# Kernel tuning notes

Hardware: AMD Instinct MI355X
Metric: run time of the kernel (lower is better)

Reference implementation:

```python
import jax, jax.numpy as jnp
import numpy as np

N, M, E, DIM, H = 50000, 50000, 640000, 128, 8
DH = DIM // H
EPS = 1e-5

def _prelu(x, alpha):
    return jnp.where(x >= 0, x, alpha * x)

def setup_inputs() -> dict:
    key0 = jax.random.key(0)
    ks = jax.random.split(key0, 12)
    s = 1.0 / np.sqrt(DIM)
    return {
        "query": jax.random.normal(ks[0], (N, DIM), jnp.float32),
        "key": jax.random.normal(ks[1], (M, DIM), jnp.float32),
        "value": jax.random.normal(ks[2], (M, DIM), jnp.float32),
        "query_idx": jax.random.randint(ks[3], (E,), 0, N),
        "key_idx": jax.random.randint(ks[4], (E,), 0, M),
        "Wq": jax.random.normal(ks[5], (DIM, DIM), jnp.float32) * s,
        "bq": jnp.zeros((DIM,), jnp.float32),
        "Wk": jax.random.normal(ks[6], (DIM, DIM), jnp.float32) * s,
        "bk": jnp.zeros((DIM,), jnp.float32),
        "Wv": jax.random.normal(ks[7], (DIM, DIM), jnp.float32) * s,
        "bv": jnp.zeros((DIM,), jnp.float32),
        "Wp": jax.random.normal(ks[8], (DIM, DIM), jnp.float32) * s,
        "bp": jnp.zeros((DIM,), jnp.float32),
        "a": jax.random.normal(ks[9], (1, H, DH), jnp.float32) * 0.1,
        "alpha": jnp.full((1,), 0.25, jnp.float32),
        "gamma": jnp.ones((DIM,), jnp.float32),
        "beta": jnp.zeros((DIM,), jnp.float32),
    }

def reference(query, key, value, query_idx, key_idx, Wq, bq, Wk, bk, Wv, bv, Wp, bp, a, alpha, gamma, beta):
    n = query.shape[0]
    # projections (node-level, then gather per edge; linear commutes with gather)
    Qq = query @ Wq + bq            # [N, DIM]
    Kq = query @ Wk + bk            # [N, DIM] (self-attn key)
    Kk = key @ Wk + bk              # [M, DIM]
    Vq = query @ Wv + bv            # [N, DIM]
    Vv = value @ Wv + bv            # [M, DIM]
    # self-attention score per query node: [N, H, 1]
    attn_qq = (a * _prelu(Qq + Kq, alpha).reshape(n, H, DH)).sum(-1, keepdims=True)
    # per-edge additive attention score: [E, H, 1]
    e_feat = _prelu(Qq[query_idx] + Kk[key_idx], alpha)
    attn_e = (a * e_feat.reshape(-1, H, DH)).sum(-1, keepdims=True)
    # stable softmax over irregular query groups (include self)
    max_attn = jax.lax.stop_gradient(attn_qq.at[query_idx].max(attn_e))
    exp_qq = jnp.exp(attn_qq - max_attn)                 # [N, H, 1]
    exp_e = jnp.exp(attn_e - max_attn[query_idx])        # [E, H, 1]
    denom = exp_qq.at[query_idx].add(exp_e)              # [N, H, 1]
    denom = jnp.where(denom == 0, 1.0, denom)
    # weighted value scatter-sum (value_idx == key_idx)
    msg = exp_qq * Vq.reshape(n, H, DH)
    msg = msg.at[query_idx].add(exp_e * Vv[key_idx].reshape(-1, H, DH))
    out = (msg / denom).reshape(n, DIM) @ Wp + bp
    res = query + out
    mu = res.mean(-1, keepdims=True)
    var = res.var(-1, keepdims=True)
    return gamma * (res - mu) / jnp.sqrt(var + EPS) + beta
```

## Files before the change

### kernel.cpp

```cpp
#include <hip/hip_runtime.h>
#include <math.h>

#define DIM 128
#define NH 8
#define LN_EPS 1e-5f
#define NEGINF -3.0e38f

using bf16x8 = __attribute__((ext_vector_type(8))) short;
using f32x4  = __attribute__((ext_vector_type(4))) float;

__device__ __forceinline__ float prelu_f(float x, float al) { return x >= 0.f ? x : al * x; }

__device__ __forceinline__ short f2bf(float f) {
    unsigned u = __float_as_uint(f);
    unsigned r = (u + 0x7fffu + ((u >> 16) & 1u)) >> 16;
    return (short)r;
}
__device__ __forceinline__ float bflo(unsigned u) { return __uint_as_float(u << 16); }
__device__ __forceinline__ float bfhi(unsigned u) { return __uint_as_float(u & 0xffff0000u); }
__device__ __forceinline__ float bfs(short s) { return __uint_as_float(((unsigned)(unsigned short)s) << 16); }

__device__ __forceinline__ unsigned cvt_pk_bf16(float lo, float hi) {
    unsigned r;
    asm("v_cvt_pk_bf16_f32 %0, %1, %2" : "=v"(r) : "v"(lo), "v"(hi));
    return r;
}

__device__ __forceinline__ float swz_xor1(float x) {
    return __int_as_float(__builtin_amdgcn_ds_swizzle(__float_as_int(x), 0x041F));
}
__device__ __forceinline__ float swz_xor16(float x) {
    return __int_as_float(__builtin_amdgcn_ds_swizzle(__float_as_int(x), 0x401F));
}
__device__ __forceinline__ float swz_xor32(float x) {
    return __shfl_xor(x, 32);
}

__global__ __launch_bounds__(256) void setup_kernel(
    const float* __restrict__ W0, const float* __restrict__ W1,
    const float* __restrict__ W2, const float* __restrict__ W3,
    short* __restrict__ P0, short* __restrict__ P1,
    short* __restrict__ P2, short* __restrict__ P3)
{
    const int id = blockIdx.x * 256 + threadIdx.x;
    const int mat = id >> 11;
    const int rem = id & 2047;
    const int ks = rem >> 9;
    const int ct = (rem >> 6) & 7;
    const int lane = rem & 63;
    const int lr = lane & 15, lg = lane >> 4;
    const float* W = mat == 0 ? W0 : mat == 1 ? W1 : mat == 2 ? W2 : W3;
    short* P = mat == 0 ? P0 : mat == 1 ? P1 : mat == 2 ? P2 : P3;
    short v[8];
    #pragma unroll
    for (int r = 0; r < 8; ++r)
        v[r] = f2bf(W[(ks * 32 + lg * 8 + r) * DIM + ct * 16 + lr]);
    *(bf16x8*)&P[(size_t)((ks * 8 + ct) * 64 + lane) * 8] = *(bf16x8*)v;
}

__global__ __launch_bounds__(256) void proj_all_mfma(
    const float* __restrict__ query,
    const float* __restrict__ key, const float* __restrict__ value,
    const short* __restrict__ Wqp, const short* __restrict__ Wkp, const short* __restrict__ Wvp,
    const float* __restrict__ bq, const float* __restrict__ bk, const float* __restrict__ bv,
    const float* __restrict__ avec, const float* __restrict__ alpha_p,
    short* __restrict__ QV16, float* __restrict__ attnqq8,
    short* __restrict__ KV16,
    const int* __restrict__ qidx, int* __restrict__ counts, int E,
    int N, int M, int nb)
{
    __shared__ short wbuf[16384];
    __shared__ short tile[4][16][132];
    const int wid = threadIdx.x >> 6, lane = threadIdx.x & 63;
    const int lr = lane & 15, lg = lane >> 4;
    const int mb = (M + 63) >> 6;

    if ((int)blockIdx.x >= nb + mb) {
        const int b = (int)blockIdx.x - nb - mb;
        for (int e = b * 256 + threadIdx.x; e < E; e += 1024 * 256)
            atomicAdd(&counts[qidx[e]], 1);
        return;
    }

    #define STAGE_W(Wsrc)                                                     \
        {                                                                     \
            _Pragma("unroll")                                                 \
            for (int j = 0; j < 8; ++j) {                                     \
                const int cch = (int)threadIdx.x + j * 256;                   \
                *(bf16x8*)&wbuf[cch * 8] = *(const bf16x8*)&(Wsrc)[cch * 8];  \
            }                                                                 \
        }

    if ((int)blockIdx.x < nb) {
        const int row0 = ((int)blockIdx.x * 4 + wid) * 16;
        const int arow = row0 + lr;
        const bool rowok = arow < N;

        bf16x8 afrag[4];
        #pragma unroll
        for (int ks = 0; ks < 4; ++ks) {
            float t[8] = {0.f,0.f,0.f,0.f,0.f,0.f,0.f,0.f};
            if (rowok) {
                *(float4*)&t[0] = *(const float4*)&query[(size_t)arow * DIM + ks * 32 + lg * 8];
                *(float4*)&t[4] = *(const float4*)&query[(size_t)arow * DIM + ks * 32 + lg * 8 + 4];
            }
            union { bf16x8 v; unsigned u[4]; } a;
            a.u[0] = cvt_pk_bf16(t[0], t[1]);
            a.u[1] = cvt_pk_bf16(t[2], t[3]);
            a.u[2] = cvt_pk_bf16(t[4], t[5]);
            a.u[3] = cvt_pk_bf16(t[6], t[7]);
            afrag[ks] = a.v;
        }
        const float al = alpha_p[0];
        unsigned* qvout = (unsigned*)QV16;

        STAGE_W(Wqp);
        __syncthreads();
        #pragma unroll 2
        for (int ct = 0; ct < 8; ++ct) {
            f32x4 aq = (f32x4)0.f;
            #pragma unroll
            for (int ks = 0; ks < 4; ++ks)
                aq = __builtin_amdgcn_mfma_f32_16x16x32_bf16(afrag[ks],
                        *(const bf16x8*)&wbuf[((ks * 8 + ct) * 64 + lane) * 8], aq, 0, 0, 0);
            const int col = ct * 16 + lr;
            const float bqv = bq[col];
            #pragma unroll
            for (int r = 0; r < 4; ++r)
                tile[wid][lg * 4 + r][col] = (short)cvt_pk_bf16(aq[r] + bqv, 0.f);
        }
        #pragma unroll
        for (int rr = 0; rr < 16; ++rr) {
            const int grow = row0 + rr;
            if (grow < N) {
                const short2 pr = *(const short2*)&tile[wid][rr][lane * 2];
                qvout[(size_t)grow * 128 + lane] =
                    (unsigned)(unsigned short)pr.x | ((unsigned)(unsigned short)pr.y << 16);
            }
        }
        __syncthreads();

        STAGE_W(Wkp);
        __syncthreads();
        #pragma unroll 2
        for (int ct = 0; ct < 8; ++ct) {
            f32x4 ak = (f32x4)0.f;
            #pragma unroll
            for (int ks = 0; ks < 4; ++ks)
                ak = __builtin_amdgcn_mfma_f32_16x16x32_bf16(afrag[ks],
                        *(const bf16x8*)&wbuf[((ks * 8 + ct) * 64 + lane) * 8], ak, 0, 0, 0);
            const int col = ct * 16 + lr;
            const float bkv = bk[col], av = avec[col];
            #pragma unroll
            for (int r = 0; r < 4; ++r) {
                const int row = lg * 4 + r;
                const float qv = bfs(tile[wid][row][col]);
                const float kv = ak[r] + bkv;
                float part = av * prelu_f(qv + kv, al);
                part += swz_xor1(part);
                const int grow = row0 + row;
                if ((lr & 1) == 0 && grow < N)
                    attnqq8[(size_t)grow * 64 + ct * 8 + (lr >> 1)] = part;
            }
        }
        __syncthreads();

        STAGE_W(Wvp);
        __syncthreads();
        #pragma unroll 2
        for (int ct = 0; ct < 8; ++ct) {
            f32x4 acv = (f32x4)0.f;
            #pragma unroll
            for (int ks = 0; ks < 4; ++ks)
                acv = __builtin_amdgcn_mfma_f32_16x16x32_bf16(afrag[ks],
                        *(const bf16x8*)&wbuf[((ks * 8 + ct) * 64 + lane) * 8], acv, 0, 0, 0);
            const int col = ct * 16 + lr;
            const float bvv = bv[col];
            #pragma unroll
            for (int r = 0; r < 4; ++r)
                tile[wid][lg * 4 + r][col] = (short)cvt_pk_bf16(acv[r] + bvv, 0.f);
        }
        #pragma unroll
        for (int rr = 0; rr < 16; ++rr) {
            const int grow = row0 + rr;
            if (grow < N) {
                const short2 pr = *(const short2*)&tile[wid][rr][lane * 2];
                qvout[(size_t)grow * 128 + 64 + lane] =
                    (unsigned)(unsigned short)pr.x | ((unsigned)(unsigned short)pr.y << 16);
            }
        }
    } else {
        const int row0 = (((int)blockIdx.x - nb) * 4 + wid) * 16;
        const int arow = row0 + lr;
        const bool rowok = arow < M;
        unsigned* kvout = (unsigned*)KV16;

        bf16x8 afK[4], afV[4];
        #pragma unroll
        for (int ks = 0; ks < 4; ++ks) {
            float tk[8] = {0.f,0.f,0.f,0.f,0.f,0.f,0.f,0.f};
            float tv[8] = {0.f,0.f,0.f,0.f,0.f,0.f,0.f,0.f};
            if (rowok) {
                *(float4*)&tk[0] = *(const float4*)&key[(size_t)arow * DIM + ks * 32 + lg * 8];
                *(float4*)&tk[4] = *(const float4*)&key[(size_t)arow * DIM + ks * 32 + lg * 8 + 4];
                *(float4*)&tv[0] = *(const float4*)&value[(size_t)arow * DIM + ks * 32 + lg * 8];
                *(float4*)&tv[4] = *(const float4*)&value[(size_t)arow * DIM + ks * 32 + lg * 8 + 4];
            }
            union { bf16x8 v; unsigned u[4]; } a, b;
            a.u[0] = cvt_pk_bf16(tk[0], tk[1]);
            a.u[1] = cvt_pk_bf16(tk[2], tk[3]);
            a.u[2] = cvt_pk_bf16(tk[4], tk[5]);
            a.u[3] = cvt_pk_bf16(tk[6], tk[7]);
            b.u[0] = cvt_pk_bf16(tv[0], tv[1]);
            b.u[1] = cvt_pk_bf16(tv[2], tv[3]);
            b.u[2] = cvt_pk_bf16(tv[4], tv[5]);
            b.u[3] = cvt_pk_bf16(tv[6], tv[7]);
            afK[ks] = a.v; afV[ks] = b.v;
        }

        STAGE_W(Wkp);
        __syncthreads();
        #pragma unroll 2
        for (int ct = 0; ct < 8; ++ct) {
            f32x4 ack = (f32x4)0.f;
            #pragma unroll
            for (int ks = 0; ks < 4; ++ks)
                ack = __builtin_amdgcn_mfma_f32_16x16x32_bf16(afK[ks],
                        *(const bf16x8*)&wbuf[((ks * 8 + ct) * 64 + lane) * 8], ack, 0, 0, 0);
            const int col = ct * 16 + lr;
            const float bkv = bk[col];
            #pragma unroll
            for (int r = 0; r < 4; ++r)
                tile[wid][lg * 4 + r][col] = (short)cvt_pk_bf16(ack[r] + bkv, 0.f);
        }
        #pragma unroll
        for (int rr = 0; rr < 16; ++rr) {
            const int grow = row0 + rr;
            if (grow < M) {
                const short2 pr = *(const short2*)&tile[wid][rr][lane * 2];
                kvout[(size_t)grow * 128 + lane] =
                    (unsigned)(unsigned short)pr.x | ((unsigned)(unsigned short)pr.y << 16);
            }
        }
        __syncthreads();

        STAGE_W(Wvp);
        __syncthreads();
        #pragma unroll 2
        for (int ct = 0; ct < 8; ++ct) {
            f32x4 acv = (f32x4)0.f;
            #pragma unroll
            for (int ks = 0; ks < 4; ++ks)
                acv = __builtin_amdgcn_mfma_f32_16x16x32_bf16(afV[ks],
                        *(const bf16x8*)&wbuf[((ks * 8 + ct) * 64 + lane) * 8], acv, 0, 0, 0);
            const int col = ct * 16 + lr;
            const float bvv = bv[col];
            #pragma unroll
            for (int r = 0; r < 4; ++r)
                tile[wid][lg * 4 + r][col] = (short)cvt_pk_bf16(acv[r] + bvv, 0.f);
        }
        #pragma unroll
        for (int rr = 0; rr < 16; ++rr) {
            const int grow = row0 + rr;
            if (grow < M) {
                const short2 pr = *(const short2*)&tile[wid][rr][lane * 2];
                kvout[(size_t)grow * 128 + 64 + lane] =
                    (unsigned)(unsigned short)pr.x | ((unsigned)(unsigned short)pr.y << 16);
            }
        }
    }
    #undef STAGE_W
}

__global__ __launch_bounds__(256) void scan1_kernel(const int* __restrict__ counts,
                                                    int* __restrict__ bsum, int N)
{
    __shared__ int sh[256];
    int i = blockIdx.x * 256 + threadIdx.x;
    sh[threadIdx.x] = (i < N) ? counts[i] : 0;
    __syncthreads();
    #pragma unroll
    for (int off = 128; off; off >>= 1) {
        if (threadIdx.x < off) sh[threadIdx.x] += sh[threadIdx.x + off];
        __syncthreads();
    }
    if (threadIdx.x == 0) bsum[blockIdx.x] = sh[0];
}

__global__ __launch_bounds__(256) void scan2_kernel(const int* __restrict__ bsum,
                                                    int* __restrict__ boff, int B)
{
    int t = threadIdx.x;
    if (B > 256) {
        if (t == 0) { int run = 0; for (int i = 0; i < B; ++i) { int v = bsum[i]; boff[i] = run; run += v; } }
        return;
    }
    __shared__ int sh[256];
    int v = (t < B) ? bsum[t] : 0;
    sh[t] = v;
    __syncthreads();
    for (int off = 1; off < 256; off <<= 1) {
        int x = (t >= off) ? sh[t - off] : 0;
        __syncthreads();
        sh[t] += x;
        __syncthreads();
    }
    if (t < B) boff[t] = sh[t] - v;
}

__global__ __launch_bounds__(256) void scan3_kernel(const int* __restrict__ counts,
                                                    const int* __restrict__ boff,
                                                    int* __restrict__ offsets,
                                                    int* __restrict__ cursor,
                                                    int N, int E)
{
    __shared__ int sh[256];
    int t = threadIdx.x;
    int i = blockIdx.x * 256 + t;
    int v = (i < N) ? counts[i] : 0;
    sh[t] = v;
    __syncthreads();
    for (int off = 1; off < 256; off <<= 1) {
        int x = (t >= off) ? sh[t - off] : 0;
        __syncthreads();
        sh[t] += x;
        __syncthreads();
    }
    int base = boff[blockIdx.x];
    if (i < N) {
        int o = base + sh[t] - v;
        offsets[i] = o;
        cursor[i] = o;
    }
    if (i == 0) offsets[N] = E;
}

__global__ void fill_kernel(const int* __restrict__ qidx, const int* __restrict__ kidx,
                            int* __restrict__ cursor, int* __restrict__ ksorted, int E)
{
    for (int e = blockIdx.x * blockDim.x + threadIdx.x; e < E; e += gridDim.x * blockDim.x) {
        int q = qidx[e];
        int pos = atomicAdd(&cursor[q], 1);
        ksorted[pos] = kidx[e];
    }
}

__global__ __launch_bounds__(256) void edge_agg_kernel(
    const short* __restrict__ QV16, const float* __restrict__ attnqq8,
    const short* __restrict__ KV16,
    const int* __restrict__ ksorted, const int* __restrict__ offsets,
    const float* __restrict__ avec, const float* __restrict__ alpha_p,
    short* __restrict__ msgn16, int N)
{
    const int lane = threadIdx.x & 63;
    const int wid  = threadIdx.x >> 6;
    const int e    = lane >> 4;
    const int sub  = lane & 15;
    const int h    = sub >> 1;

    const float al = alpha_p[0];
    const float r  = (1.f - al) / (1.f + al);
    const float s1 = (1.f + al) * 0.5f;

    float c[8];
    {
        const float4 a0 = *(const float4*)&avec[sub * 8];
        const float4 a1 = *(const float4*)&avec[sub * 8 + 4];
        c[0] = a0.x * s1; c[1] = a0.y * s1; c[2] = a0.z * s1; c[3] = a0.w * s1;
        c[4] = a1.x * s1; c[5] = a1.y * s1; c[6] = a1.z * s1; c[7] = a1.w * s1;
    }

    const char* KVb = (const char*)KV16;
    const unsigned subB = (unsigned)(sub * 16);
    const int wavesTotal = gridDim.x * 4;

    for (int n = blockIdx.x * 4 + wid; n < N; n += wavesTotal) {
        float q[8];
        {
            unsigned qd[4];
            *(uint4*)qd = *(const uint4*)&QV16[(size_t)n * 256 + sub * 8];
            #pragma unroll
            for (int j = 0; j < 4; ++j) { q[2*j] = bflo(qd[j]); q[2*j+1] = bfhi(qd[j]); }
        }

        float acc[8];
        float den;
        if (e == 0) {
            float sself;
            {
                const float4 a4 = *(const float4*)&attnqq8[(size_t)n * 64 + h * 8];
                const float4 b4 = *(const float4*)&attnqq8[(size_t)n * 64 + h * 8 + 4];
                sself = ((a4.x + a4.y) + (a4.z + a4.w)) + ((b4.x + b4.y) + (b4.z + b4.w));
            }
            const float ws = __expf(sself);
            unsigned vdi[4];
            *(uint4*)vdi = *(const uint4*)&QV16[(size_t)n * 256 + 128 + sub * 8];
            #pragma unroll
            for (int j = 0; j < 4; ++j) {
                acc[2*j]   = ws * bflo(vdi[j]);
                acc[2*j+1] = ws * bfhi(vdi[j]);
            }
            den = ws;
        } else {
            #pragma unroll
            for (int d = 0; d < 8; ++d) acc[d] = 0.f;
            den = 0.f;
        }

        const int p0 = offsets[n];
        const int p1 = offsets[n + 1];
        const int T  = (p1 - p0 + 3) >> 2;

        #define ROWLOAD(kd_, vd_, ki_)                                        \
            {                                                                 \
                const unsigned ob = (unsigned)(ki_) * 512u + subB;            \
                *(uint4*)(kd_) = *(const uint4*)(KVb + ob);                   \
                *(uint4*)(vd_) = *(const uint4*)(KVb + ob + 256);             \
            }

        unsigned kdA[4], vdA[4], kdB[4], vdB[4];
        unsigned kdC[4], vdC[4], kdD[4], vdD[4];
        bool vA, vB, vC, vD;
        int kiA, kiB, kiC, kiD;

        {
            int i0 = p0 + e,      i1 = p0 + 4 + e;
            int i2 = p0 + 8 + e,  i3 = p0 + 12 + e;
            vA = i0 < p1; vB = i1 < p1; vC = i2 < p1; vD = i3 < p1;
            const int k0 = vA ? ksorted[i0] : 0;
            const int k1 = vB ? ksorted[i1] : 0;
            const int k2 = vC ? ksorted[i2] : 0;
            const int k3 = vD ? ksorted[i3] : 0;
            ROWLOAD(kdA, vdA, k0); ROWLOAD(kdB, vdB, k1);
            ROWLOAD(kdC, vdC, k2); ROWLOAD(kdD, vdD, k3);
            int j0 = p0 + 16 + e, j1 = p0 + 20 + e;
            int j2 = p0 + 24 + e, j3 = p0 + 28 + e;
            kiA = (j0 < p1) ? ksorted[j0] : 0;
            kiB = (j1 < p1) ? ksorted[j1] : 0;
            kiC = (j2 < p1) ? ksorted[j2] : 0;
            kiD = (j3 < p1) ? ksorted[j3] : 0;
        }

        #define COMPUTE(kd_, vd_, vflag)                                      \
            {                                                                 \
                float sp = 0.f;                                               \
                _Pragma("unroll")                                             \
                for (int j = 0; j < 4; ++j) {                                 \
                    const float x0 = q[2*j]   + bflo(kd_[j]);                 \
                    const float x1 = q[2*j+1] + bfhi(kd_[j]);                 \
                    const float t0 = fmaf(r, __builtin_fabsf(x0), x0);        \
                    const float t1 = fmaf(r, __builtin_fabsf(x1), x1);        \
                    sp = fmaf(c[2*j], t0, sp);                                \
                    sp = fmaf(c[2*j+1], t1, sp);                              \
                }                                                             \
                const float sf = sp + swz_xor1(sp);                           \
                const float s = (vflag) ? sf : NEGINF;                        \
                const float w = __expf(s);                 \
                den += w;                                                     \
                _Pragma("unroll")                                             \
                for (int j = 0; j < 4; ++j) {                                 \
                    acc[2*j]   = fmaf(w, bflo(vd_[j]), acc[2*j]);             \
                    acc[2*j+1] = fmaf(w, bfhi(vd_[j]), acc[2*j+1]);           \
                }                                                             \
            }

        #define RELOAD(kd_, vd_, vflag, ki_, st4, st8)                        \
            {                                                                 \
                vflag = (p0 + (st4) * 4 + e) < p1;                            \
                ROWLOAD(kd_, vd_, ki_);                                       \
                const int fi = p0 + (st8) * 4 + e;                            \
                ki_ = (fi < p1) ? ksorted[fi] : 0;                            \
            }

        #pragma unroll 1
        for (int t = 0; t < T; t += 4) {
            COMPUTE(kdA, vdA, vA); RELOAD(kdA, vdA, vA, kiA, t + 4, t + 8);
            COMPUTE(kdB, vdB, vB); RELOAD(kdB, vdB, vB, kiB, t + 5, t + 9);
            COMPUTE(kdC, vdC, vC); RELOAD(kdC, vdC, vC, kiC, t + 6, t + 10);
            COMPUTE(kdD, vdD, vD); RELOAD(kdD, vdD, vD, kiD, t + 7, t + 11);
        }
        #undef COMPUTE
        #undef RELOAD
        #undef ROWLOAD

        {
            den += swz_xor16(den);
            #pragma unroll
            for (int d = 0; d < 8; ++d) acc[d] += swz_xor16(acc[d]);
            den += swz_xor32(den);
            #pragma unroll
            for (int d = 0; d < 8; ++d) acc[d] += swz_xor32(acc[d]);
        }

        if (e == 0) {
            const float inv = 1.f / den;
            unsigned u[4];
            #pragma unroll
            for (int j = 0; j < 4; ++j)
                u[j] = cvt_pk_bf16(acc[2*j] * inv, acc[2*j+1] * inv);
            *(uint4*)&msgn16[(size_t)n * DIM + sub * 8] = *(uint4*)u;
        }
    }
}

__global__ __launch_bounds__(256) void out_ln_mfma(
    const short* __restrict__ msgn16, const short* __restrict__ Wpp,
    const float* __restrict__ bp, const float* __restrict__ query,
    const float* __restrict__ gamma, const float* __restrict__ beta,
    float* __restrict__ out, int N)
{
    __shared__ float ys[64][130];
    const int wid = threadIdx.x >> 6, lane = threadIdx.x & 63;
    const int rowbase = blockIdx.x * 64;
    const int row0 = rowbase + wid * 16;
    const int lr = lane & 15, lg = lane >> 4;

    if (row0 < N) {
        bf16x8 afrag[4];
        const int arow = row0 + lr;
        const bool rowok = arow < N;
        #pragma unroll
        for (int ks = 0; ks < 4; ++ks) {
            if (rowok)
                afrag[ks] = *(const bf16x8*)&msgn16[(size_t)arow * DIM + ks * 32 + lg * 8];
            else {
                bf16x8 z;
                #pragma unroll
                for (int j = 0; j < 8; ++j) z[j] = 0;
                afrag[ks] = z;
            }
        }
        #pragma unroll 2
        for (int ct = 0; ct < 8; ++ct) {
            f32x4 acc = (f32x4)0.f;
            #pragma unroll
            for (int ks = 0; ks < 4; ++ks) {
                const size_t bo = (size_t)((ks * 8 + ct) * 64 + lane) * 8;
                acc = __builtin_amdgcn_mfma_f32_16x16x32_bf16(afrag[ks], *(const bf16x8*)&Wpp[bo], acc, 0, 0, 0);
            }
            const int col = ct * 16 + lr;
            const float bpv = bp[col];
            #pragma unroll
            for (int r = 0; r < 4; ++r)
                ys[wid * 16 + lg * 4 + r][col] = acc[r] + bpv;
        }
    }
    __syncthreads();

    for (int rr = 0; rr < 16; ++rr) {
        const int r = wid * 16 + rr;
        const int grow = rowbase + r;
        if (grow >= N) break;
        const float y1 = ys[r][lane], y2 = ys[r][lane + 64];
        const float q1 = query[(size_t)grow * DIM + lane];
        const float q2 = query[(size_t)grow * DIM + lane + 64];
        const float r1 = y1 + q1, r2 = y2 + q2;
        float s = r1 + r2;
        float ss = r1 * r1 + r2 * r2;
        #pragma unroll
        for (int off = 32; off; off >>= 1) {
            s += __shfl_xor(s, off);
            ss += __shfl_xor(ss, off);
        }
        const float mu = s * (1.f / DIM);
        const float var = ss * (1.f / DIM) - mu * mu;
        const float rstd = rsqrtf(var + LN_EPS);
        out[(size_t)grow * DIM + lane] = gamma[lane] * (r1 - mu) * rstd + beta[lane];
        out[(size_t)grow * DIM + lane + 64] = gamma[lane + 64] * (r2 - mu) * rstd + beta[lane + 64];
    }
}

extern "C" void kernel_launch(void* const* d_in, const int* in_sizes, int n_in,
                              void* d_out, int out_size, void* d_ws, size_t ws_size,
                              hipStream_t stream) {
    const float* query = (const float*)d_in[0];
    const float* key   = (const float*)d_in[1];
    const float* value = (const float*)d_in[2];
    const int* query_idx = (const int*)d_in[3];
    const int* key_idx   = (const int*)d_in[4];
    const float* Wq = (const float*)d_in[5];
    const float* bq = (const float*)d_in[6];
    const float* Wk = (const float*)d_in[7];
    const float* bk = (const float*)d_in[8];
    const float* Wv = (const float*)d_in[9];
    const float* bv = (const float*)d_in[10];
    const float* Wp = (const float*)d_in[11];
    const float* bp = (const float*)d_in[12];
    const float* avec  = (const float*)d_in[13];
    const float* alpha = (const float*)d_in[14];
    const float* gamma = (const float*)d_in[15];
    const float* beta  = (const float*)d_in[16];
    float* out = (float*)d_out;

    const int N = in_sizes[0] / DIM;
    const int M = in_sizes[1] / DIM;
    const int E = in_sizes[3];

    float* f = (float*)d_ws;
    float* attnqq8 = f; f += (size_t)N * 64;
    short* sp = (short*)f;
    short* QV16 = sp;   sp += (size_t)N * 256;
    short* KV16 = sp;   sp += (size_t)M * 256;
    short* msgn16 = sp; sp += (size_t)N * DIM;
    short* Wqp = sp;    sp += DIM * DIM;
    short* Wkp = sp;    sp += DIM * DIM;
    short* Wvp = sp;    sp += DIM * DIM;
    short* Wpp = sp;    sp += DIM * DIM;
    int* ip = (int*)(((size_t)sp + 15) & ~(size_t)15);
    int* counts  = ip;  ip += N;
    int* offsets = ip;  ip += N + 1;
    int* cursor  = ip;  ip += N;
    int* bsum    = ip;  ip += 4096;
    int* boff    = ip;  ip += 4096;
    int* ksorted = ip;  ip += E;

    const int B = (N + 255) / 256;
    const int nb = (N + 63) / 64;
    const int mb = (M + 63) / 64;

    hipMemsetAsync(counts, 0, (size_t)N * sizeof(int), stream);

    setup_kernel<<<32, 256, 0, stream>>>(Wq, Wk, Wv, Wp, Wqp, Wkp, Wvp, Wpp);

    proj_all_mfma<<<nb + mb + 1024, 256, 0, stream>>>(
        query, key, value, Wqp, Wkp, Wvp, bq, bk, bv, avec, alpha,
        QV16, attnqq8, KV16, query_idx, counts, E, N, M, nb);

    scan1_kernel<<<B, 256, 0, stream>>>(counts, bsum, N);
    scan2_kernel<<<1, 256, 0, stream>>>(bsum, boff, B);
    scan3_kernel<<<B, 256, 0, stream>>>(counts, boff, offsets, cursor, N, E);
    fill_kernel<<<1024, 256, 0, stream>>>(query_idx, key_idx, cursor, ksorted, E);

    edge_agg_kernel<<<2048, 256, 0, stream>>>(
        QV16, attnqq8, KV16, ksorted, offsets, avec, alpha, msgn16, N);

    out_ln_mfma<<<(N + 63) / 64, 256, 0, stream>>>(
        msgn16, Wpp, bp, query, gamma, beta, out, N);
}
```

Baseline: 192.1 us.

## Persistent projection blocks with per-block weight staging; move count atomics to setup

The projection kernel now runs a fixed grid of 384+384 persistent blocks. Each block stages a weight matrix into LDS once and loops over many 64-row tiles, where previously every tile restaged all three matrices. The query-side Wq·Wk self-attention score now writes the Kq projection to a scratch buffer (msgn16, reused before edge_agg writes it) and reads it back in the Q pass. The edge-count atomics move into the setup kernel, and the projection launch moves after the scan/fill kernels. This reduces weight staging traffic but reloads the input rows once per weight pass and adds a global scratch round trip.

```diff
diff --git a/kernel.cpp b/kernel.cpp
--- a/kernel.cpp
+++ b/kernel.cpp
@@ -18,7 +18,7 @@
 }
 __device__ __forceinline__ float bflo(unsigned u) { return __uint_as_float(u << 16); }
 __device__ __forceinline__ float bfhi(unsigned u) { return __uint_as_float(u & 0xffff0000u); }
-__device__ __forceinline__ float bfs(short s) { return __uint_as_float(((unsigned)(unsigned short)s) << 16); }
+__device__ __forceinline__ float bfus(unsigned short s) { return __uint_as_float(((unsigned)s) << 16); }
 
 __device__ __forceinline__ unsigned cvt_pk_bf16(float lo, float hi) {
     unsigned r;
@@ -40,22 +40,29 @@
     const float* __restrict__ W0, const float* __restrict__ W1,
     const float* __restrict__ W2, const float* __restrict__ W3,
     short* __restrict__ P0, short* __restrict__ P1,
-    short* __restrict__ P2, short* __restrict__ P3)
-{
-    const int id = blockIdx.x * 256 + threadIdx.x;
-    const int mat = id >> 11;
-    const int rem = id & 2047;
-    const int ks = rem >> 9;
-    const int ct = (rem >> 6) & 7;
-    const int lane = rem & 63;
-    const int lr = lane & 15, lg = lane >> 4;
-    const float* W = mat == 0 ? W0 : mat == 1 ? W1 : mat == 2 ? W2 : W3;
-    short* P = mat == 0 ? P0 : mat == 1 ? P1 : mat == 2 ? P2 : P3;
-    short v[8];
-    #pragma unroll
-    for (int r = 0; r < 8; ++r)
-        v[r] = f2bf(W[(ks * 32 + lg * 8 + r) * DIM + ct * 16 + lr]);
-    *(bf16x8*)&P[(size_t)((ks * 8 + ct) * 64 + lane) * 8] = *(bf16x8*)v;
+    short* __restrict__ P2, short* __restrict__ P3,
+    const int* __restrict__ qidx, int* __restrict__ counts, int E)
+{
+    if (blockIdx.x < 32) {
+        const int id = blockIdx.x * 256 + threadIdx.x;
+        const int mat = id >> 11;
+        const int rem = id & 2047;
+        const int ks = rem >> 9;
+        const int ct = (rem >> 6) & 7;
+        const int lane = rem & 63;
+        const int lr = lane & 15, lg = lane >> 4;
+        const float* W = mat == 0 ? W0 : mat == 1 ? W1 : mat == 2 ? W2 : W3;
+        short* P = mat == 0 ? P0 : mat == 1 ? P1 : mat == 2 ? P2 : P3;
+        short v[8];
+        #pragma unroll
+        for (int r = 0; r < 8; ++r)
+            v[r] = f2bf(W[(ks * 32 + lg * 8 + r) * DIM + ct * 16 + lr]);
+        *(bf16x8*)&P[(size_t)((ks * 8 + ct) * 64 + lane) * 8] = *(bf16x8*)v;
+    } else {
+        const int b = blockIdx.x - 32;
+        for (int e = b * 256 + threadIdx.x; e < E; e += 1024 * 256)
+            atomicAdd(&counts[qidx[e]], 1);
+    }
 }
 
 __global__ __launch_bounds__(256) void proj_all_mfma(
@@ -65,22 +72,15 @@
     const float* __restrict__ bq, const float* __restrict__ bk, const float* __restrict__ bv,
     const float* __restrict__ avec, const float* __restrict__ alpha_p,
     short* __restrict__ QV16, float* __restrict__ attnqq8,
-    short* __restrict__ KV16,
-    const int* __restrict__ qidx, int* __restrict__ counts, int E,
-    int N, int M, int nb)
+    short* __restrict__ KV16, short* __restrict__ Kscr,
+    int N, int M, int QB, int KB)
 {
     __shared__ short wbuf[16384];
     __shared__ short tile[4][16][132];
     const int wid = threadIdx.x >> 6, lane = threadIdx.x & 63;
     const int lr = lane & 15, lg = lane >> 4;
-    const int mb = (M + 63) >> 6;
-
-    if ((int)blockIdx.x >= nb + mb) {
-        const int b = (int)blockIdx.x - nb - mb;
-        for (int e = b * 256 + threadIdx.x; e < E; e += 1024 * 256)
-            atomicAdd(&counts[qidx[e]], 1);
-        return;
-    }
+    const int nTN = (N + 63) >> 6;
+    const int nTM = (M + 63) >> 6;
 
     #define STAGE_W(Wsrc)                                                     \
         {                                                                     \
@@ -91,185 +91,196 @@
             }                                                                 \
         }
 
-    if ((int)blockIdx.x < nb) {
-        const int row0 = ((int)blockIdx.x * 4 + wid) * 16;
-        const int arow = row0 + lr;
-        const bool rowok = arow < N;
-
-        bf16x8 afrag[4];
-        #pragma unroll
-        for (int ks = 0; ks < 4; ++ks) {
-            float t[8] = {0.f,0.f,0.f,0.f,0.f,0.f,0.f,0.f};
-            if (rowok) {
-                *(float4*)&t[0] = *(const float4*)&query[(size_t)arow * DIM + ks * 32 + lg * 8];
-                *(float4*)&t[4] = *(const float4*)&query[(size_t)arow * DIM + ks * 32 + lg * 8 + 4];
-            }
-            union { bf16x8 v; unsigned u[4]; } a;
-            a.u[0] = cvt_pk_bf16(t[0], t[1]);
-            a.u[1] = cvt_pk_bf16(t[2], t[3]);
-            a.u[2] = cvt_pk_bf16(t[4], t[5]);
-            a.u[3] = cvt_pk_bf16(t[6], t[7]);
-            afrag[ks] = a.v;
-        }
+    #define LOAD_AFRAG(src, limit)                                            \
+        {                                                                     \
+            const int arow = row0 + lr;                                       \
+            const bool rowok = arow < (limit);                                \
+            _Pragma("unroll")                                                 \
+            for (int ks = 0; ks < 4; ++ks) {                                  \
+                float t_[8] = {0.f,0.f,0.f,0.f,0.f,0.f,0.f,0.f};              \
+                if (rowok) {                                                  \
+                    *(float4*)&t_[0] = *(const float4*)&(src)[(size_t)arow * DIM + ks * 32 + lg * 8];     \
+                    *(float4*)&t_[4] = *(const float4*)&(src)[(size_t)arow * DIM + ks * 32 + lg * 8 + 4]; \
+                }                                                             \
+                union { bf16x8 v; unsigned u[4]; } a_;                        \
+                a_.u[0] = cvt_pk_bf16(t_[0], t_[1]);                          \
+                a_.u[1] = cvt_pk_bf16(t_[2], t_[3]);                          \
+                a_.u[2] = cvt_pk_bf16(t_[4], t_[5]);                          \
+                a_.u[3] = cvt_pk_bf16(t_[6], t_[7]);                          \
+                afrag[ks] = a_.v;                                             \
+            }                                                                 \
+        }
+
+    if ((int)blockIdx.x < QB) {
         const float al = alpha_p[0];
         unsigned* qvout = (unsigned*)QV16;
+        unsigned* kscro = (unsigned*)Kscr;
+        bf16x8 afrag[4];
+
+        STAGE_W(Wkp);
+        __syncthreads();
+        for (int t = blockIdx.x; t < nTN; t += QB) {
+            const int row0 = t * 64 + wid * 16;
+            LOAD_AFRAG(query, N);
+            #pragma unroll 2
+            for (int ct = 0; ct < 8; ++ct) {
+                f32x4 ak = (f32x4)0.f;
+                #pragma unroll
+                for (int ks = 0; ks < 4; ++ks)
+                    ak = __builtin_amdgcn_mfma_f32_16x16x32_bf16(afrag[ks],
+                            *(const bf16x8*)&wbuf[((ks * 8 + ct) * 64 + lane) * 8], ak, 0, 0, 0);
+                const int col = ct * 16 + lr;
+                const float bkv = bk[col];
+                #pragma unroll
+                for (int r = 0; r < 4; ++r)
+                    tile[wid][lg * 4 + r][col] = (short)cvt_pk_bf16(ak[r] + bkv, 0.f);
+            }
+            #pragma unroll
+            for (int rr = 0; rr < 16; ++rr) {
+                const int grow = row0 + rr;
+                if (grow < N) {
+                    const short2 pr = *(const short2*)&tile[wid][rr][lane * 2];
+                    kscro[(size_t)grow * 64 + lane] =
+                        (unsigned)(unsigned short)pr.x | ((unsigned)(unsigned short)pr.y << 16);
+                }
+            }
+        }
+        __syncthreads();
 
         STAGE_W(Wqp);
         __syncthreads();
-        #pragma unroll 2
-        for (int ct = 0; ct < 8; ++ct) {
-            f32x4 aq = (f32x4)0.f;
-            #pragma unroll
-            for (int ks = 0; ks < 4; ++ks)
-                aq = __builtin_amdgcn_mfma_f32_16x16x32_bf16(afrag[ks],
-                        *(const bf16x8*)&wbuf[((ks * 8 + ct) * 64 + lane) * 8], aq, 0, 0, 0);
-            const int col = ct * 16 + lr;
-            const float bqv = bq[col];
-            #pragma unroll
-            for (int r = 0; r < 4; ++r)
-                tile[wid][lg * 4 + r][col] = (short)cvt_pk_bf16(aq[r] + bqv, 0.f);
-        }
-        #pragma unroll
-        for (int rr = 0; rr < 16; ++rr) {
-            const int grow = row0 + rr;
-            if (grow < N) {
-                const short2 pr = *(const short2*)&tile[wid][rr][lane * 2];
-                qvout[(size_t)grow * 128 + lane] =
-                    (unsigned)(unsigned short)pr.x | ((unsigned)(unsigned short)pr.y << 16);
-            }
-        }
-        __syncthreads();
+        for (int t = blockIdx.x; t < nTN; t += QB) {
+            const int row0 = t * 64 + wid * 16;
+            LOAD_AFRAG(query, N);
+            #pragma unroll 2
+            for (int ct = 0; ct < 8; ++ct) {
+                f32x4 aq = (f32x4)0.f;
+                #pragma unroll
+                for (int ks = 0; ks < 4; ++ks)
+                    aq = __builtin_amdgcn_mfma_f32_16x16x32_bf16(afrag[ks],
+                            *(const bf16x8*)&wbuf[((ks * 8 + ct) * 64 + lane) * 8], aq, 0, 0, 0);
+                const int col = ct * 16 + lr;
+                const float bqv = bq[col], av = avec[col];
+                #pragma unroll
+                for (int r = 0; r < 4; ++r) {
+                    const int row = lg * 4 + r;
+                    const int grow = row0 + row;
+                    const float qv = aq[r] + bqv;
+                    const float kvb = (grow < N)
+                        ? bfus(((const unsigned short*)Kscr)[(size_t)grow * 128 + col]) : 0.f;
+                    float part = av * prelu_f(qv + kvb, al);
+                    part += swz_xor1(part);
+                    if ((lr & 1) == 0 && grow < N)
+                        attnqq8[(size_t)grow * 64 + ct * 8 + (lr >> 1)] = part;
+                    tile[wid][row][col] = (short)cvt_pk_bf16(qv, 0.f);
+                }
+            }
+            #pragma unroll
+            for (int rr = 0; rr < 16; ++rr) {
+                const int grow = row0 + rr;
+                if (grow < N) {
+                    const short2 pr = *(const short2*)&tile[wid][rr][lane * 2];
+                    qvout[(size_t)grow * 128 + lane] =
+                        (unsigned)(unsigned short)pr.x | ((unsigned)(unsigned short)pr.y << 16);
+                }
+            }
+        }
+        __syncthreads();
+
+        STAGE_W(Wvp);
+        __syncthreads();
+        for (int t = blockIdx.x; t < nTN; t += QB) {
+            const int row0 = t * 64 + wid * 16;
+            LOAD_AFRAG(query, N);
+            #pragma unroll 2
+            for (int ct = 0; ct < 8; ++ct) {
+                f32x4 acv = (f32x4)0.f;
+                #pragma unroll
+                for (int ks = 0; ks < 4; ++ks)
+                    acv = __builtin_amdgcn_mfma_f32_16x16x32_bf16(afrag[ks],
+                            *(const bf16x8*)&wbuf[((ks * 8 + ct) * 64 + lane) * 8], acv, 0, 0, 0);
+                const int col = ct * 16 + lr;
+                const float bvv = bv[col];
+                #pragma unroll
+                for (int r = 0; r < 4; ++r)
+                    tile[wid][lg * 4 + r][col] = (short)cvt_pk_bf16(acv[r] + bvv, 0.f);
+            }
+            #pragma unroll
+            for (int rr = 0; rr < 16; ++rr) {
+                const int grow = row0 + rr;
+                if (grow < N) {
+                    const short2 pr = *(const short2*)&tile[wid][rr][lane * 2];
+                    qvout[(size_t)grow * 128 + 64 + lane] =
+                        (unsigned)(unsigned short)pr.x | ((unsigned)(unsigned short)pr.y << 16);
+                }
+            }
+        }
+    } else {
+        const int b = (int)blockIdx.x - QB;
+        unsigned* kvout = (unsigned*)KV16;
+        bf16x8 afrag[4];
 
         STAGE_W(Wkp);
         __syncthreads();
-        #pragma unroll 2
-        for (int ct = 0; ct < 8; ++ct) {
-            f32x4 ak = (f32x4)0.f;
-            #pragma unroll
-            for (int ks = 0; ks < 4; ++ks)
-                ak = __builtin_amdgcn_mfma_f32_16x16x32_bf16(afrag[ks],
-                        *(const bf16x8*)&wbuf[((ks * 8 + ct) * 64 + lane) * 8], ak, 0, 0, 0);
-            const int col = ct * 16 + lr;
-            const float bkv = bk[col], av = avec[col];
-            #pragma unroll
-            for (int r = 0; r < 4; ++r) {
-                const int row = lg * 4 + r;
-                const float qv = bfs(tile[wid][row][col]);
-                const float kv = ak[r] + bkv;
-                float part = av * prelu_f(qv + kv, al);
-                part += swz_xor1(part);
-                const int grow = row0 + row;
-                if ((lr & 1) == 0 && grow < N)
-                    attnqq8[(size_t)grow * 64 + ct * 8 + (lr >> 1)] = part;
+        for (int t = b; t < nTM; t += KB) {
+            const int row0 = t * 64 + wid * 16;
+            LOAD_AFRAG(key, M);
+            #pragma unroll 2
+            for (int ct = 0; ct < 8; ++ct) {
+                f32x4 ack = (f32x4)0.f;
+                #pragma unroll
+                for (int ks = 0; ks < 4; ++ks)
+                    ack = __builtin_amdgcn_mfma_f32_16x16x32_bf16(afrag[ks],
+                            *(const bf16x8*)&wbuf[((ks * 8 + ct) * 64 + lane) * 8], ack, 0, 0, 0);
+                const int col = ct * 16 + lr;
+                const float bkv = bk[col];
+                #pragma unroll
+                for (int r = 0; r < 4; ++r)
+                    tile[wid][lg * 4 + r][col] = (short)cvt_pk_bf16(ack[r] + bkv, 0.f);
+            }
+            #pragma unroll
+            for (int rr = 0; rr < 16; ++rr) {
+                const int grow = row0 + rr;
+                if (grow < M) {
+                    const short2 pr = *(const short2*)&tile[wid][rr][lane * 2];
+                    kvout[(size_t)grow * 128 + lane] =
+                        (unsigned)(unsigned short)pr.x | ((unsigned)(unsigned short)pr.y << 16);
+                }
             }
         }
         __syncthreads();
 
         STAGE_W(Wvp);
         __syncthreads();
-        #pragma unroll 2
-        for (int ct = 0; ct < 8; ++ct) {
-            f32x4 acv = (f32x4)0.f;
-            #pragma unroll
-            for (int ks = 0; ks < 4; ++ks)
-                acv = __builtin_amdgcn_mfma_f32_16x16x32_bf16(afrag[ks],
-                        *(const bf16x8*)&wbuf[((ks * 8 + ct) * 64 + lane) * 8], acv, 0, 0, 0);
-            const int col = ct * 16 + lr;
-            const float bvv = bv[col];
-            #pragma unroll
-            for (int r = 0; r < 4; ++r)
-                tile[wid][lg * 4 + r][col] = (short)cvt_pk_bf16(acv[r] + bvv, 0.f);
-        }
-        #pragma unroll
-        for (int rr = 0; rr < 16; ++rr) {
-            const int grow = row0 + rr;
-            if (grow < N) {
-                const short2 pr = *(const short2*)&tile[wid][rr][lane * 2];
-                qvout[(size_t)grow * 128 + 64 + lane] =
-                    (unsigned)(unsigned short)pr.x | ((unsigned)(unsigned short)pr.y << 16);
-            }
-        }
-    } else {
-        const int row0 = (((int)blockIdx.x - nb) * 4 + wid) * 16;
-        const int arow = row0 + lr;
-        const bool rowok = arow < M;
-        unsigned* kvout = (unsigned*)KV16;
-
-        bf16x8 afK[4], afV[4];
-        #pragma unroll
-        for (int ks = 0; ks < 4; ++ks) {
-            float tk[8] = {0.f,0.f,0.f,0.f,0.f,0.f,0.f,0.f};
-            float tv[8] = {0.f,0.f,0.f,0.f,0.f,0.f,0.f,0.f};
-            if (rowok) {
-                *(float4*)&tk[0] = *(const float4*)&key[(size_t)arow * DIM + ks * 32 + lg * 8];
-                *(float4*)&tk[4] = *(const float4*)&key[(size_t)arow * DIM + ks * 32 + lg * 8 + 4];
-                *(float4*)&tv[0] = *(const float4*)&value[(size_t)arow * DIM + ks * 32 + lg * 8];
-                *(float4*)&tv[4] = *(const float4*)&value[(size_t)arow * DIM + ks * 32 + lg * 8 + 4];
-            }
-            union { bf16x8 v; unsigned u[4]; } a, b;
-            a.u[0] = cvt_pk_bf16(tk[0], tk[1]);
-            a.u[1] = cvt_pk_bf16(tk[2], tk[3]);
-            a.u[2] = cvt_pk_bf16(tk[4], tk[5]);
-            a.u[3] = cvt_pk_bf16(tk[6], tk[7]);
-            b.u[0] = cvt_pk_bf16(tv[0], tv[1]);
-            b.u[1] = cvt_pk_bf16(tv[2], tv[3]);
-            b.u[2] = cvt_pk_bf16(tv[4], tv[5]);
-            b.u[3] = cvt_pk_bf16(tv[6], tv[7]);
-            afK[ks] = a.v; afV[ks] = b.v;
-        }
-
-        STAGE_W(Wkp);
-        __syncthreads();
-        #pragma unroll 2
-        for (int ct = 0; ct < 8; ++ct) {
-            f32x4 ack = (f32x4)0.f;
-            #pragma unroll
-            for (int ks = 0; ks < 4; ++ks)
-                ack = __builtin_amdgcn_mfma_f32_16x16x32_bf16(afK[ks],
-                        *(const bf16x8*)&wbuf[((ks * 8 + ct) * 64 + lane) * 8], ack, 0, 0, 0);
-            const int col = ct * 16 + lr;
-            const float bkv = bk[col];
-            #pragma unroll
-            for (int r = 0; r < 4; ++r)
-                tile[wid][lg * 4 + r][col] = (short)cvt_pk_bf16(ack[r] + bkv, 0.f);
-        }
-        #pragma unroll
-        for (int rr = 0; rr < 16; ++rr) {
-            const int grow = row0 + rr;
-            if (grow < M) {
-                const short2 pr = *(const short2*)&tile[wid][rr][lane * 2];
-                kvout[(size_t)grow * 128 + lane] =
-                    (unsigned)(unsigned short)pr.x | ((unsigned)(unsigned short)pr.y << 16);
-            }
-        }
-        __syncthreads();
-
-        STAGE_W(Wvp);
-        __syncthreads();
-        #pragma unroll 2
-        for (int ct = 0; ct < 8; ++ct) {
-            f32x4 acv = (f32x4)0.f;
-            #pragma unroll
-            for (int ks = 0; ks < 4; ++ks)
-                acv = __builtin_amdgcn_mfma_f32_16x16x32_bf16(afV[ks],
-                        *(const bf16x8*)&wbuf[((ks * 8 + ct) * 64 + lane) * 8], acv, 0, 0, 0);
-            const int col = ct * 16 + lr;
-            const float bvv = bv[col];
-            #pragma unroll
-            for (int r = 0; r < 4; ++r)
-                tile[wid][lg * 4 + r][col] = (short)cvt_pk_bf16(acv[r] + bvv, 0.f);
-        }
-        #pragma unroll
-        for (int rr = 0; rr < 16; ++rr) {
-            const int grow = row0 + rr;
-            if (grow < M) {
-                const short2 pr = *(const short2*)&tile[wid][rr][lane * 2];
-                kvout[(size_t)grow * 128 + 64 + lane] =
-                    (unsigned)(unsigned short)pr.x | ((unsigned)(unsigned short)pr.y << 16);
+        for (int t = b; t < nTM; t += KB) {
+            const int row0 = t * 64 + wid * 16;
+            LOAD_AFRAG(value, M);
+            #pragma unroll 2
+            for (int ct = 0; ct < 8; ++ct) {
+                f32x4 acv = (f32x4)0.f;
+                #pragma unroll
+                for (int ks = 0; ks < 4; ++ks)
+                    acv = __builtin_amdgcn_mfma_f32_16x16x32_bf16(afrag[ks],
+                            *(const bf16x8*)&wbuf[((ks * 8 + ct) * 64 + lane) * 8], acv, 0, 0, 0);
+                const int col = ct * 16 + lr;
+                const float bvv = bv[col];
+                #pragma unroll
+                for (int r = 0; r < 4; ++r)
+                    tile[wid][lg * 4 + r][col] = (short)cvt_pk_bf16(acv[r] + bvv, 0.f);
+            }
+            #pragma unroll
+            for (int rr = 0; rr < 16; ++rr) {
+                const int grow = row0 + rr;
+                if (grow < M) {
+                    const short2 pr = *(const short2*)&tile[wid][rr][lane * 2];
+                    kvout[(size_t)grow * 128 + 64 + lane] =
+                        (unsigned)(unsigned short)pr.x | ((unsigned)(unsigned short)pr.y << 16);
+                }
             }
         }
     }
     #undef STAGE_W
+    #undef LOAD_AFRAG
 }
 
 __global__ __launch_bounds__(256) void scan1_kernel(const int* __restrict__ counts,
@@ -615,22 +626,22 @@
     int* ksorted = ip;  ip += E;
 
     const int B = (N + 255) / 256;
-    const int nb = (N + 63) / 64;
-    const int mb = (M + 63) / 64;
+    const int QB = 384, KB = 384;
 
     hipMemsetAsync(counts, 0, (size_t)N * sizeof(int), stream);
 
-    setup_kernel<<<32, 256, 0, stream>>>(Wq, Wk, Wv, Wp, Wqp, Wkp, Wvp, Wpp);
-
-    proj_all_mfma<<<nb + mb + 1024, 256, 0, stream>>>(
-        query, key, value, Wqp, Wkp, Wvp, bq, bk, bv, avec, alpha,
-        QV16, attnqq8, KV16, query_idx, counts, E, N, M, nb);
+    setup_kernel<<<1056, 256, 0, stream>>>(Wq, Wk, Wv, Wp, Wqp, Wkp, Wvp, Wpp,
+                                           query_idx, counts, E);
 
     scan1_kernel<<<B, 256, 0, stream>>>(counts, bsum, N);
     scan2_kernel<<<1, 256, 0, stream>>>(bsum, boff, B);
     scan3_kernel<<<B, 256, 0, stream>>>(counts, boff, offsets, cursor, N, E);
     fill_kernel<<<1024, 256, 0, stream>>>(query_idx, key_idx, cursor, ksorted, E);
 
+    proj_all_mfma<<<QB + KB, 256, 0, stream>>>(
+        query, key, value, Wqp, Wkp, Wvp, bq, bk, bv, avec, alpha,
+        QV16, attnqq8, KV16, msgn16, N, M, QB, KB);
+
     edge_agg_kernel<<<2048, 256, 0, stream>>>(
         QV16, attnqq8, KV16, ksorted, offsets, avec, alpha, msgn16, N);
 
```

New measurement: 229.2 us. +19.3%, slower.
